# Performance work log

Measured on AMD Instinct MI355X. Metric: run time of the kernel, lower is better.

Reference implementation:

```python
import jax, jax.numpy as jnp
import numpy as np

B, H, T, D = 2, 16, 2048, 64


def setup_inputs() -> dict:
    key = jax.random.key(0)
    kq, kk, kv, km = jax.random.split(key, 4)
    q = jax.random.normal(kq, (B, H, T, D), dtype=jnp.float32)
    k = jax.random.normal(kk, (B, H, T, D), dtype=jnp.float32)
    v = jax.random.normal(kv, (B, H, T, D), dtype=jnp.float32)
    # boolean mask, True = masked out (broadcast over batch and heads)
    mask = jax.random.randint(km, (1, 1, T, T), 0, 2).astype(jnp.bool_)
    return {"q": q, "k": k, "v": v, "mask": mask}


def reference(q, k, v, mask):
    scale = q.shape[-1] ** (-0.5)
    # [B,H,T,T] score matrix (materialized, as in the original)
    scores = jnp.einsum("bhqd,bhkd->bhqk", q, k) * scale
    scores = jnp.where(mask, jnp.float32(-10000.0), scores)
    attn = jax.nn.softmax(scores, axis=-1)
    attn = jnp.where(mask, jnp.float32(0.0), attn)
    return jnp.einsum("bhqk,bhkd->bhqd", attn, v)
```

## Files before the change

kernel.cpp:

```cpp
#include <hip/hip_runtime.h>
#include <hip/hip_bf16.h>

typedef __bf16 bf16x8 __attribute__((ext_vector_type(8)));
typedef __bf16 bf16x4 __attribute__((ext_vector_type(4)));
typedef float  f32x4  __attribute__((ext_vector_type(4)));

#define T_SEQ 2048
#define D_HEAD 64
#define BH_N 32
#define NT_TILES (T_SEQ / 64)
#define QT_N 16
#define IMG_BYTES 16384
#define SCALE_LOG2 0.18033688011112042f

#define WS_IMG ((size_t)0)
#define WS_MB  ((size_t)16u << 20)

static __device__ __forceinline__ f32x4 mfma32(bf16x8 a, bf16x8 b, f32x4 c) {
    return __builtin_amdgcn_mfma_f32_16x16x32_bf16(a, b, c, 0, 0, 0);
}

static __device__ __forceinline__ float fast_exp2(float x) {
#if __has_builtin(__builtin_amdgcn_exp2f)
    return __builtin_amdgcn_exp2f(x);
#else
    return exp2f(x);
#endif
}

static __device__ __forceinline__ void gload16(const void* g, void* l, int lane) {
#if __has_builtin(__builtin_amdgcn_global_load_lds)
    (void)lane;
    __builtin_amdgcn_global_load_lds(
        (const __attribute__((address_space(1))) void*)g,
        (__attribute__((address_space(3))) void*)l, 16, 0, 0);
#else
    *((f32x4*)l + lane) = *(const f32x4*)g;
#endif
}


__global__ __launch_bounds__(256) void prep_kv(const float* __restrict__ k,
                                               const float* __restrict__ v,
                                               char* __restrict__ img) {
    __shared__ __bf16 t[64][72];
    const int bh = blockIdx.y, tt = blockIdx.x, tid = threadIdx.x;
    char* ob = img + ((size_t)bh * NT_TILES + tt) * IMG_BYTES;
    {
        const int kr = tid >> 2, qd = tid & 3, ke = kr & 7;
        const size_t base = ((size_t)bh * T_SEQ + tt * 64 + kr) * D_HEAD + qd * 16;
        const float4 a0 = *(const float4*)(k + base);
        const float4 a1 = *(const float4*)(k + base + 4);
        const float4 a2 = *(const float4*)(k + base + 8);
        const float4 a3 = *(const float4*)(k + base + 12);
        bf16x8 w0, w1;
        w0[0]=(__bf16)a0.x; w0[1]=(__bf16)a0.y; w0[2]=(__bf16)a0.z; w0[3]=(__bf16)a0.w;
        w0[4]=(__bf16)a1.x; w0[5]=(__bf16)a1.y; w0[6]=(__bf16)a1.z; w0[7]=(__bf16)a1.w;
        w1[0]=(__bf16)a2.x; w1[1]=(__bf16)a2.y; w1[2]=(__bf16)a2.z; w1[3]=(__bf16)a2.w;
        w1[4]=(__bf16)a3.x; w1[5]=(__bf16)a3.y; w1[6]=(__bf16)a3.z; w1[7]=(__bf16)a3.w;
        *(bf16x8*)(ob + kr * 128 + (((2 * qd + 0) ^ ke) << 4)) = w0;
        *(bf16x8*)(ob + kr * 128 + (((2 * qd + 1) ^ ke) << 4)) = w1;
    }
    {
        const int tr = tid >> 4, c4 = (tid & 15) * 4;
        const float* src = v + ((size_t)bh * T_SEQ + tt * 64) * D_HEAD;
#pragma unroll
        for (int p = 0; p < 4; ++p) {
            const int row = p * 16 + tr;
            const float4 f = *(const float4*)(src + row * D_HEAD + c4);
            t[c4+0][row] = (__bf16)f.x; t[c4+1][row] = (__bf16)f.y;
            t[c4+2][row] = (__bf16)f.z; t[c4+3][row] = (__bf16)f.w;
        }
        __syncthreads();
        const int d = tid >> 2;
        char* vb = ob + 8192 + d * 128;
#pragma unroll
        for (int mi = 0; mi < 2; ++mi) {
            const int m  = (tid & 3) * 2 + mi;
            const int u  = m ^ (d & 7);
            const int k0 = (u & 1) * 32 + (u >> 1) * 4;
            const bf16x4 lo = *(const bf16x4*)&t[d][k0];
            const bf16x4 hi = *(const bf16x4*)&t[d][k0 + 16];
            *(bf16x8*)(vb + m * 16) = __builtin_shufflevector(lo, hi, 0,1,2,3,4,5,6,7);
        }
    }
}

__global__ void mpack(const int* __restrict__ m, unsigned long long* __restrict__ mb) {
    const int i = blockIdx.x * 256 + threadIdx.x;
    const unsigned long long b = __ballot(m[i] != 0);
    if ((threadIdx.x & 63) == 0) mb[i >> 6] = b;
}


__global__ __launch_bounds__(512, 4) void attn11(
    const float* __restrict__ q, const char* __restrict__ img,
    const unsigned long long* __restrict__ mb, float* __restrict__ out)
{
    const int l   = blockIdx.x;
    const int m_  = l >> 3;
    const int bh  = ((l & 7) << 2) | (m_ & 3);
    const int qt  = m_ >> 2;

    const int tid = threadIdx.x, wave = tid >> 6, lane = tid & 63;
    const int g = lane >> 4, ln = lane & 15;
    const int qp = wave & 3, kh = wave >> 2;

    __shared__ __align__(16) char smem[33280];
    float* Ep = (float*)smem;
    float* Os = (float*)(smem + 32768);

    const int qw = qt * 128 + qp * 32;

    bf16x8 qf[2][2];
#pragma unroll
    for (int qs = 0; qs < 2; ++qs) {
        const float* qpt = q + ((size_t)bh * T_SEQ + qw + qs * 16 + ln) * D_HEAD + g * 8;
#pragma unroll
        for (int kc = 0; kc < 2; ++kc) {
            const float4 f0 = *(const float4*)(qpt + kc * 32);
            const float4 f1 = *(const float4*)(qpt + kc * 32 + 4);
            qf[qs][kc][0]=(__bf16)(f0.x*SCALE_LOG2); qf[qs][kc][1]=(__bf16)(f0.y*SCALE_LOG2);
            qf[qs][kc][2]=(__bf16)(f0.z*SCALE_LOG2); qf[qs][kc][3]=(__bf16)(f0.w*SCALE_LOG2);
            qf[qs][kc][4]=(__bf16)(f1.x*SCALE_LOG2); qf[qs][kc][5]=(__bf16)(f1.y*SCALE_LOG2);
            qf[qs][kc][6]=(__bf16)(f1.z*SCALE_LOG2); qf[qs][kc][7]=(__bf16)(f1.w*SCALE_LOG2);
        }
    }

    f32x4 o[2][4];
#pragma unroll
    for (int qs = 0; qs < 2; ++qs)
#pragma unroll
        for (int mt = 0; mt < 4; ++mt) o[qs][mt] = (f32x4){0.f, 0.f, 0.f, 0.f};
    f32x4 osum[2] = { (f32x4){0.f,0.f,0.f,0.f}, (f32x4){0.f,0.f,0.f,0.f} };
    const bf16x8 ones8 = { (__bf16)1.0f, (__bf16)1.0f, (__bf16)1.0f, (__bf16)1.0f,
                           (__bf16)1.0f, (__bf16)1.0f, (__bf16)1.0f, (__bf16)1.0f };

    const char* ibase = img + (size_t)bh * (NT_TILES * (size_t)IMG_BYTES);
    const unsigned long long* mrow0 = mb + (size_t)(qw + ln) * 32;
    const unsigned long long* mrow1 = mb + (size_t)(qw + 16 + ln) * 32;

    int koffs[2][2];
#pragma unroll
    for (int ntl = 0; ntl < 2; ++ntl) {
        const int row = (2 * kh + ntl) * 16 + ln;
        const int rb = row * 128 + ((g ^ (ln & 7)) << 4);
        koffs[ntl][0] = rb; koffs[ntl][1] = rb ^ 64;
    }
    int voffs[4];
#pragma unroll
    for (int mt = 0; mt < 4; ++mt)
        voffs[mt] = (mt * 16 + ln) * 128 + ((((g << 1) | kh) ^ (ln & 7)) << 4);

    char* buf0 = smem;
    char* buf1 = smem + 16384;

    auto stage = [&](int tile, char* dstbase) {
        const char* src = ibase + (size_t)tile * IMG_BYTES + wave * 2048 + lane * 16;
        char* dst = dstbase + wave * 2048;
        gload16(src, dst, lane);
        gload16(src + 1024, dst + 1024, lane);
    };

    auto compute_tile = [&](const char* KB, const char* VB,
                            unsigned long long w0, unsigned long long w1) {
        const unsigned nbs0 = (~(unsigned)(w0 >> (kh << 5))) >> (g * 4);
        const unsigned nbs1 = (~(unsigned)(w1 >> (kh << 5))) >> (g * 4);

        bf16x8 ka[2][2];
#pragma unroll
        for (int ntl = 0; ntl < 2; ++ntl) {
            ka[ntl][0] = *(const bf16x8*)(KB + koffs[ntl][0]);
            ka[ntl][1] = *(const bf16x8*)(KB + koffs[ntl][1]);
        }

        bf16x8 pa8[2];
#pragma unroll
        for (int ntl = 0; ntl < 2; ++ntl) {
#pragma unroll
            for (int qs = 0; qs < 2; ++qs) {
                f32x4 c = (f32x4){0.f, 0.f, 0.f, 0.f};
                __builtin_amdgcn_s_setprio(1);
                c = mfma32(ka[ntl][0], qf[qs][0], c);
                c = mfma32(ka[ntl][1], qf[qs][1], c);
                __builtin_amdgcn_s_setprio(0);
                const unsigned nbs = qs ? nbs1 : nbs0;
#pragma unroll
                for (int r = 0; r < 4; ++r) {
                    const float e = fast_exp2(c[r]);
                    const int keep = (int)(nbs << (31 - (ntl * 16 + r))) >> 31;
                    const float p = __builtin_bit_cast(float,
                        __builtin_bit_cast(unsigned, e) & (unsigned)keep);
                    pa8[qs][ntl * 4 + r] = (__bf16)p;
                }
            }
        }

        bf16x8 vv[4];
#pragma unroll
        for (int mt = 0; mt < 4; ++mt) vv[mt] = *(const bf16x8*)(VB + voffs[mt]);
        __builtin_amdgcn_s_setprio(1);
#pragma unroll
        for (int qs = 0; qs < 2; ++qs) osum[qs] = mfma32(pa8[qs], ones8, osum[qs]);
#pragma unroll
        for (int mt = 0; mt < 4; ++mt)
#pragma unroll
            for (int qs = 0; qs < 2; ++qs)
                o[qs][mt] = mfma32(pa8[qs], vv[mt], o[qs][mt]);
        __builtin_amdgcn_s_setprio(0);
    };

    stage(0, buf0);
    unsigned long long mwA0 = mrow0[0], mwA1 = mrow1[0];
    __syncthreads();

#pragma unroll 1
    for (int i = 0; i < NT_TILES / 2; ++i) {
        const int t = 2 * i;
        stage(t + 1, buf1);
        const unsigned long long mwB0 = mrow0[t + 1], mwB1 = mrow1[t + 1];
        compute_tile(buf0, buf0 + 8192, mwA0, mwA1);
        __syncthreads();
        if (i < NT_TILES / 2 - 1) {
            stage(t + 2, buf0);
            mwA0 = mrow0[t + 2]; mwA1 = mrow1[t + 2];
        }
        compute_tile(buf1, buf1 + 8192, mwB0, mwB1);
        __syncthreads();
    }

#pragma unroll
    for (int pass = 0; pass < 2; ++pass) {
        if ((qp >> 1) == pass) {
            const int qpl = qp & 1;
#pragma unroll
            for (int qs = 0; qs < 2; ++qs) {
#pragma unroll
                for (int mt = 0; mt < 4; ++mt)
#pragma unroll
                    for (int r = 0; r < 4; ++r)
                        Ep[(size_t)kh * 4096 + (qpl * 32 + qs * 16 + g * 4 + r) * 64 + mt * 16 + ln] = o[qs][mt][r];
                if (ln == 0) {
#pragma unroll
                    for (int r = 0; r < 4; ++r)
                        Os[kh * 64 + qpl * 32 + qs * 16 + g * 4 + r] = osum[qs][r];
                }
            }
        }
        __syncthreads();
#pragma unroll
        for (int p2 = 0; p2 < 2; ++p2) {
            const int idx = p2 * 512 + tid;
            const int row = idx >> 4, c4 = (idx & 15) * 4;
            const float sl = Os[row] + Os[64 + row];
            const float inv = (sl > 0.f) ? (1.f / sl) : 0.f;
            const float4 a  = *(const float4*)(Ep + row * 64 + c4);
            const float4 b4 = *(const float4*)(Ep + 4096 + row * 64 + c4);
            const float4 st = { (a.x + b4.x) * inv, (a.y + b4.y) * inv,
                                (a.z + b4.z) * inv, (a.w + b4.w) * inv };
            *(float4*)(out + ((size_t)bh * T_SEQ + qt * 128 + pass * 64 + row) * D_HEAD + c4) = st;
        }
        if (pass == 0) __syncthreads();
    }
}

extern "C" void kernel_launch(void* const* d_in, const int* in_sizes, int n_in,
                              void* d_out, int out_size, void* d_ws, size_t ws_size,
                              hipStream_t stream) {
    const float* q    = (const float*)d_in[0];
    const float* k    = (const float*)d_in[1];
    const float* v    = (const float*)d_in[2];
    const int*   mask = (const int*)d_in[3];
    float*       out  = (float*)d_out;

    char* img = (char*)d_ws + WS_IMG;
    unsigned long long* mbw = (unsigned long long*)((char*)d_ws + WS_MB);

    prep_kv<<<dim3(NT_TILES, BH_N), 256, 0, stream>>>(k, v, img);
    mpack<<<(T_SEQ * T_SEQ) / 256, 256, 0, stream>>>(mask, mbw);
    attn11<<<dim3(QT_N * BH_N), 512, 0, stream>>>(q, img, mbw, out);
}
```

Measured before the change: 159.5 us.

## Halve query rows per block to double grid size and cut register use

Each block now processes 64 query rows instead of 128, with one 16-row query slice per wave, and the grid doubles. This halves per-wave accumulator and Q-fragment registers and raises the occupancy hint to 8 blocks per CU, aiming for more parallelism and better latency hiding. In exchange, each K/V tile is loaded from global memory and staged into LDS twice as often per output, and each loaded K fragment is reused across fewer MFMAs. The epilogue becomes a single pass.

```diff
diff --git a/kernel.cpp b/kernel.cpp
--- a/kernel.cpp
+++ b/kernel.cpp
@@ -9,7 +9,7 @@
 #define D_HEAD 64
 #define BH_N 32
 #define NT_TILES (T_SEQ / 64)
-#define QT_N 16
+#define QT_N 32
 #define IMG_BYTES 16384
 #define SCALE_LOG2 0.18033688011112042f
 
@@ -93,14 +93,13 @@
 }
 
 
-__global__ __launch_bounds__(512, 4) void attn11(
+__global__ __launch_bounds__(512, 8) void attn12(
     const float* __restrict__ q, const char* __restrict__ img,
     const unsigned long long* __restrict__ mb, float* __restrict__ out)
 {
     const int l   = blockIdx.x;
-    const int m_  = l >> 3;
-    const int bh  = ((l & 7) << 2) | (m_ & 3);
-    const int qt  = m_ >> 2;
+    const int bh  = ((l & 7) << 2) | ((l >> 3) & 3);
+    const int qt  = l >> 5;
 
     const int tid = threadIdx.x, wave = tid >> 6, lane = tid & 63;
     const int g = lane >> 4, ln = lane & 15;
@@ -110,35 +109,31 @@
     float* Ep = (float*)smem;
     float* Os = (float*)(smem + 32768);
 
-    const int qw = qt * 128 + qp * 32;
-
-    bf16x8 qf[2][2];
-#pragma unroll
-    for (int qs = 0; qs < 2; ++qs) {
-        const float* qpt = q + ((size_t)bh * T_SEQ + qw + qs * 16 + ln) * D_HEAD + g * 8;
+    const int qw = qt * 64 + qp * 16;
+
+    bf16x8 qf[2];
+    {
+        const float* qpt = q + ((size_t)bh * T_SEQ + qw + ln) * D_HEAD + g * 8;
 #pragma unroll
         for (int kc = 0; kc < 2; ++kc) {
             const float4 f0 = *(const float4*)(qpt + kc * 32);
             const float4 f1 = *(const float4*)(qpt + kc * 32 + 4);
-            qf[qs][kc][0]=(__bf16)(f0.x*SCALE_LOG2); qf[qs][kc][1]=(__bf16)(f0.y*SCALE_LOG2);
-            qf[qs][kc][2]=(__bf16)(f0.z*SCALE_LOG2); qf[qs][kc][3]=(__bf16)(f0.w*SCALE_LOG2);
-            qf[qs][kc][4]=(__bf16)(f1.x*SCALE_LOG2); qf[qs][kc][5]=(__bf16)(f1.y*SCALE_LOG2);
-            qf[qs][kc][6]=(__bf16)(f1.z*SCALE_LOG2); qf[qs][kc][7]=(__bf16)(f1.w*SCALE_LOG2);
-        }
-    }
-
-    f32x4 o[2][4];
-#pragma unroll
-    for (int qs = 0; qs < 2; ++qs)
-#pragma unroll
-        for (int mt = 0; mt < 4; ++mt) o[qs][mt] = (f32x4){0.f, 0.f, 0.f, 0.f};
-    f32x4 osum[2] = { (f32x4){0.f,0.f,0.f,0.f}, (f32x4){0.f,0.f,0.f,0.f} };
+            qf[kc][0]=(__bf16)(f0.x*SCALE_LOG2); qf[kc][1]=(__bf16)(f0.y*SCALE_LOG2);
+            qf[kc][2]=(__bf16)(f0.z*SCALE_LOG2); qf[kc][3]=(__bf16)(f0.w*SCALE_LOG2);
+            qf[kc][4]=(__bf16)(f1.x*SCALE_LOG2); qf[kc][5]=(__bf16)(f1.y*SCALE_LOG2);
+            qf[kc][6]=(__bf16)(f1.z*SCALE_LOG2); qf[kc][7]=(__bf16)(f1.w*SCALE_LOG2);
+        }
+    }
+
+    f32x4 o[4];
+#pragma unroll
+    for (int mt = 0; mt < 4; ++mt) o[mt] = (f32x4){0.f, 0.f, 0.f, 0.f};
+    f32x4 osum = (f32x4){0.f, 0.f, 0.f, 0.f};
     const bf16x8 ones8 = { (__bf16)1.0f, (__bf16)1.0f, (__bf16)1.0f, (__bf16)1.0f,
                            (__bf16)1.0f, (__bf16)1.0f, (__bf16)1.0f, (__bf16)1.0f };
 
     const char* ibase = img + (size_t)bh * (NT_TILES * (size_t)IMG_BYTES);
-    const unsigned long long* mrow0 = mb + (size_t)(qw + ln) * 32;
-    const unsigned long long* mrow1 = mb + (size_t)(qw + 16 + ln) * 32;
+    const unsigned long long* mrow = mb + (size_t)(qw + ln) * 32;
 
     int koffs[2][2];
 #pragma unroll
@@ -162,105 +157,80 @@
         gload16(src + 1024, dst + 1024, lane);
     };
 
-    auto compute_tile = [&](const char* KB, const char* VB,
-                            unsigned long long w0, unsigned long long w1) {
-        const unsigned nbs0 = (~(unsigned)(w0 >> (kh << 5))) >> (g * 4);
-        const unsigned nbs1 = (~(unsigned)(w1 >> (kh << 5))) >> (g * 4);
-
-        bf16x8 ka[2][2];
+    auto compute_tile = [&](const char* KB, const char* VB, unsigned long long w0) {
+        const unsigned nbs = (~(unsigned)(w0 >> (kh << 5))) >> (g * 4);
+
+        bf16x8 pa8;
 #pragma unroll
         for (int ntl = 0; ntl < 2; ++ntl) {
-            ka[ntl][0] = *(const bf16x8*)(KB + koffs[ntl][0]);
-            ka[ntl][1] = *(const bf16x8*)(KB + koffs[ntl][1]);
-        }
-
-        bf16x8 pa8[2];
-#pragma unroll
-        for (int ntl = 0; ntl < 2; ++ntl) {
-#pragma unroll
-            for (int qs = 0; qs < 2; ++qs) {
-                f32x4 c = (f32x4){0.f, 0.f, 0.f, 0.f};
-                __builtin_amdgcn_s_setprio(1);
-                c = mfma32(ka[ntl][0], qf[qs][0], c);
-                c = mfma32(ka[ntl][1], qf[qs][1], c);
-                __builtin_amdgcn_s_setprio(0);
-                const unsigned nbs = qs ? nbs1 : nbs0;
-#pragma unroll
-                for (int r = 0; r < 4; ++r) {
-                    const float e = fast_exp2(c[r]);
-                    const int keep = (int)(nbs << (31 - (ntl * 16 + r))) >> 31;
-                    const float p = __builtin_bit_cast(float,
-                        __builtin_bit_cast(unsigned, e) & (unsigned)keep);
-                    pa8[qs][ntl * 4 + r] = (__bf16)p;
-                }
+            const bf16x8 a0 = *(const bf16x8*)(KB + koffs[ntl][0]);
+            const bf16x8 a1 = *(const bf16x8*)(KB + koffs[ntl][1]);
+            f32x4 c = (f32x4){0.f, 0.f, 0.f, 0.f};
+            __builtin_amdgcn_s_setprio(1);
+            c = mfma32(a0, qf[0], c);
+            c = mfma32(a1, qf[1], c);
+            __builtin_amdgcn_s_setprio(0);
+#pragma unroll
+            for (int r = 0; r < 4; ++r) {
+                const float e = fast_exp2(c[r]);
+                const int keep = (int)(nbs << (31 - (ntl * 16 + r))) >> 31;
+                const float p = __builtin_bit_cast(float,
+                    __builtin_bit_cast(unsigned, e) & (unsigned)keep);
+                pa8[ntl * 4 + r] = (__bf16)p;
             }
         }
 
-        bf16x8 vv[4];
-#pragma unroll
-        for (int mt = 0; mt < 4; ++mt) vv[mt] = *(const bf16x8*)(VB + voffs[mt]);
         __builtin_amdgcn_s_setprio(1);
-#pragma unroll
-        for (int qs = 0; qs < 2; ++qs) osum[qs] = mfma32(pa8[qs], ones8, osum[qs]);
-#pragma unroll
-        for (int mt = 0; mt < 4; ++mt)
-#pragma unroll
-            for (int qs = 0; qs < 2; ++qs)
-                o[qs][mt] = mfma32(pa8[qs], vv[mt], o[qs][mt]);
+        osum = mfma32(pa8, ones8, osum);
+#pragma unroll
+        for (int mt = 0; mt < 4; ++mt) {
+            const bf16x8 vv = *(const bf16x8*)(VB + voffs[mt]);
+            o[mt] = mfma32(pa8, vv, o[mt]);
+        }
         __builtin_amdgcn_s_setprio(0);
     };
 
     stage(0, buf0);
-    unsigned long long mwA0 = mrow0[0], mwA1 = mrow1[0];
+    unsigned long long mwA = mrow[0];
     __syncthreads();
 
 #pragma unroll 1
     for (int i = 0; i < NT_TILES / 2; ++i) {
         const int t = 2 * i;
         stage(t + 1, buf1);
-        const unsigned long long mwB0 = mrow0[t + 1], mwB1 = mrow1[t + 1];
-        compute_tile(buf0, buf0 + 8192, mwA0, mwA1);
+        const unsigned long long mwB = mrow[t + 1];
+        compute_tile(buf0, buf0 + 8192, mwA);
         __syncthreads();
         if (i < NT_TILES / 2 - 1) {
             stage(t + 2, buf0);
-            mwA0 = mrow0[t + 2]; mwA1 = mrow1[t + 2];
-        }
-        compute_tile(buf1, buf1 + 8192, mwB0, mwB1);
+            mwA = mrow[t + 2];
+        }
+        compute_tile(buf1, buf1 + 8192, mwB);
         __syncthreads();
     }
 
 #pragma unroll
-    for (int pass = 0; pass < 2; ++pass) {
-        if ((qp >> 1) == pass) {
-            const int qpl = qp & 1;
-#pragma unroll
-            for (int qs = 0; qs < 2; ++qs) {
-#pragma unroll
-                for (int mt = 0; mt < 4; ++mt)
-#pragma unroll
-                    for (int r = 0; r < 4; ++r)
-                        Ep[(size_t)kh * 4096 + (qpl * 32 + qs * 16 + g * 4 + r) * 64 + mt * 16 + ln] = o[qs][mt][r];
-                if (ln == 0) {
-#pragma unroll
-                    for (int r = 0; r < 4; ++r)
-                        Os[kh * 64 + qpl * 32 + qs * 16 + g * 4 + r] = osum[qs][r];
-                }
-            }
-        }
-        __syncthreads();
-#pragma unroll
-        for (int p2 = 0; p2 < 2; ++p2) {
-            const int idx = p2 * 512 + tid;
-            const int row = idx >> 4, c4 = (idx & 15) * 4;
-            const float sl = Os[row] + Os[64 + row];
-            const float inv = (sl > 0.f) ? (1.f / sl) : 0.f;
-            const float4 a  = *(const float4*)(Ep + row * 64 + c4);
-            const float4 b4 = *(const float4*)(Ep + 4096 + row * 64 + c4);
-            const float4 st = { (a.x + b4.x) * inv, (a.y + b4.y) * inv,
-                                (a.z + b4.z) * inv, (a.w + b4.w) * inv };
-            *(float4*)(out + ((size_t)bh * T_SEQ + qt * 128 + pass * 64 + row) * D_HEAD + c4) = st;
-        }
-        if (pass == 0) __syncthreads();
+    for (int mt = 0; mt < 4; ++mt)
+#pragma unroll
+        for (int r = 0; r < 4; ++r)
+            Ep[(size_t)kh * 4096 + (qp * 16 + g * 4 + r) * 64 + mt * 16 + ln] = o[mt][r];
+    if (ln == 0) {
+#pragma unroll
+        for (int r = 0; r < 4; ++r)
+            Os[kh * 64 + qp * 16 + g * 4 + r] = osum[r];
+    }
+    __syncthreads();
+#pragma unroll
+    for (int p2 = 0; p2 < 2; ++p2) {
+        const int idx = p2 * 512 + tid;
+        const int row = idx >> 4, c4 = (idx & 15) * 4;
+        const float sl = Os[row] + Os[64 + row];
+        const float inv = (sl > 0.f) ? (1.f / sl) : 0.f;
+        const float4 a  = *(const float4*)(Ep + row * 64 + c4);
+        const float4 b4 = *(const float4*)(Ep + 4096 + row * 64 + c4);
+        const float4 st = { (a.x + b4.x) * inv, (a.y + b4.y) * inv,
+                            (a.z + b4.z) * inv, (a.w + b4.w) * inv };
+        *(float4*)(out + ((size_t)bh * T_SEQ + qt * 64 + row) * D_HEAD + c4) = st;
     }
 }
 
@@ -278,5 +248,5 @@
 
     prep_kv<<<dim3(NT_TILES, BH_N), 256, 0, stream>>>(k, v, img);
     mpack<<<(T_SEQ * T_SEQ) / 256, 256, 0, stream>>>(mask, mbw);
-    attn11<<<dim3(QT_N * BH_N), 512, 0, stream>>>(q, img, mbw, out);
-}
+    attn12<<<dim3(QT_N * BH_N), 512, 0, stream>>>(q, img, mbw, out);
+}
```

After: 166.2 us. 1.04x slower.

## Software-pipeline PV matmul of previous tile with QK and softmax of current tile

Applied to the files above, without the earlier changes.

Splits the per-tile compute into QK, softmax, V-read and PV stages and reorders them so the PV MFMAs of the previous tile are issued right after the QK MFMAs of the current tile. This is meant to let exp/mask ALU work overlap MFMA execution, hiding dependency latency within a wave. It keeps the probabilities and V fragments live across iterations, which raises register pressure under the 4-waves launch bound and adds a prologue and epilogue.

```diff
diff --git a/kernel.cpp b/kernel.cpp
--- a/kernel.cpp
+++ b/kernel.cpp
@@ -93,7 +93,7 @@
 }
 
 
-__global__ __launch_bounds__(512, 4) void attn11(
+__global__ __launch_bounds__(512, 4) void attn13(
     const float* __restrict__ q, const char* __restrict__ img,
     const unsigned long long* __restrict__ mb, float* __restrict__ out)
 {
@@ -155,6 +155,9 @@
     char* buf0 = smem;
     char* buf1 = smem + 16384;
 
+    bf16x8 pa8_p[2];
+    bf16x8 vv_p[4];
+
     auto stage = [&](int tile, char* dstbase) {
         const char* src = ibase + (size_t)tile * IMG_BYTES + wave * 2048 + lane * 16;
         char* dst = dstbase + wave * 2048;
@@ -162,72 +165,109 @@
         gload16(src + 1024, dst + 1024, lane);
     };
 
-    auto compute_tile = [&](const char* KB, const char* VB,
-                            unsigned long long w0, unsigned long long w1) {
+    auto QK = [&](const char* KB, f32x4 (&c)[2][2]) {
+#pragma unroll
+        for (int ntl = 0; ntl < 2; ++ntl) {
+            const bf16x8 a0 = *(const bf16x8*)(KB + koffs[ntl][0]);
+            const bf16x8 a1 = *(const bf16x8*)(KB + koffs[ntl][1]);
+            __builtin_amdgcn_s_setprio(1);
+#pragma unroll
+            for (int qs = 0; qs < 2; ++qs) {
+                f32x4 t0 = (f32x4){0.f, 0.f, 0.f, 0.f};
+                t0 = mfma32(a0, qf[qs][0], t0);
+                t0 = mfma32(a1, qf[qs][1], t0);
+                c[ntl][qs] = t0;
+            }
+            __builtin_amdgcn_s_setprio(0);
+        }
+    };
+
+    auto PVV = [&]() {
+        __builtin_amdgcn_s_setprio(1);
+#pragma unroll
+        for (int qs = 0; qs < 2; ++qs) osum[qs] = mfma32(pa8_p[qs], ones8, osum[qs]);
+#pragma unroll
+        for (int mt = 0; mt < 4; ++mt)
+#pragma unroll
+            for (int qs = 0; qs < 2; ++qs)
+                o[qs][mt] = mfma32(pa8_p[qs], vv_p[mt], o[qs][mt]);
+        __builtin_amdgcn_s_setprio(0);
+    };
+
+    auto SOFT = [&](const f32x4 (&c)[2][2], unsigned long long w0, unsigned long long w1) {
         const unsigned nbs0 = (~(unsigned)(w0 >> (kh << 5))) >> (g * 4);
         const unsigned nbs1 = (~(unsigned)(w1 >> (kh << 5))) >> (g * 4);
-
-        bf16x8 ka[2][2];
-#pragma unroll
-        for (int ntl = 0; ntl < 2; ++ntl) {
-            ka[ntl][0] = *(const bf16x8*)(KB + koffs[ntl][0]);
-            ka[ntl][1] = *(const bf16x8*)(KB + koffs[ntl][1]);
-        }
-
-        bf16x8 pa8[2];
-#pragma unroll
-        for (int ntl = 0; ntl < 2; ++ntl) {
+#pragma unroll
+        for (int ntl = 0; ntl < 2; ++ntl)
 #pragma unroll
             for (int qs = 0; qs < 2; ++qs) {
-                f32x4 c = (f32x4){0.f, 0.f, 0.f, 0.f};
-                __builtin_amdgcn_s_setprio(1);
-                c = mfma32(ka[ntl][0], qf[qs][0], c);
-                c = mfma32(ka[ntl][1], qf[qs][1], c);
-                __builtin_amdgcn_s_setprio(0);
                 const unsigned nbs = qs ? nbs1 : nbs0;
 #pragma unroll
                 for (int r = 0; r < 4; ++r) {
-                    const float e = fast_exp2(c[r]);
+                    const float e = fast_exp2(c[ntl][qs][r]);
                     const int keep = (int)(nbs << (31 - (ntl * 16 + r))) >> 31;
                     const float p = __builtin_bit_cast(float,
                         __builtin_bit_cast(unsigned, e) & (unsigned)keep);
-                    pa8[qs][ntl * 4 + r] = (__bf16)p;
+                    pa8_p[qs][ntl * 4 + r] = (__bf16)p;
                 }
             }
-        }
-
-        bf16x8 vv[4];
-#pragma unroll
-        for (int mt = 0; mt < 4; ++mt) vv[mt] = *(const bf16x8*)(VB + voffs[mt]);
-        __builtin_amdgcn_s_setprio(1);
-#pragma unroll
-        for (int qs = 0; qs < 2; ++qs) osum[qs] = mfma32(pa8[qs], ones8, osum[qs]);
-#pragma unroll
-        for (int mt = 0; mt < 4; ++mt)
-#pragma unroll
-            for (int qs = 0; qs < 2; ++qs)
-                o[qs][mt] = mfma32(pa8[qs], vv[mt], o[qs][mt]);
-        __builtin_amdgcn_s_setprio(0);
+    };
+
+    auto VREAD = [&](const char* KB) {
+        const char* VB = KB + 8192;
+#pragma unroll
+        for (int mt = 0; mt < 4; ++mt) vv_p[mt] = *(const bf16x8*)(VB + voffs[mt]);
     };
 
     stage(0, buf0);
-    unsigned long long mwA0 = mrow0[0], mwA1 = mrow1[0];
     __syncthreads();
 
+    {
+        stage(1, buf1);
+        const unsigned long long w0 = mrow0[0], w1 = mrow1[0];
+        f32x4 c[2][2];
+        QK(buf0, c);
+        SOFT(c, w0, w1);
+        VREAD(buf0);
+        __syncthreads();
+    }
+
 #pragma unroll 1
-    for (int i = 0; i < NT_TILES / 2; ++i) {
-        const int t = 2 * i;
-        stage(t + 1, buf1);
-        const unsigned long long mwB0 = mrow0[t + 1], mwB1 = mrow1[t + 1];
-        compute_tile(buf0, buf0 + 8192, mwA0, mwA1);
+    for (int i = 0; i < 15; ++i) {
+        {
+            const int t = 2 * i + 1;
+            stage(t + 1, buf0);
+            const unsigned long long w0 = mrow0[t], w1 = mrow1[t];
+            f32x4 c[2][2];
+            QK(buf1, c);
+            PVV();
+            SOFT(c, w0, w1);
+            VREAD(buf1);
+            __syncthreads();
+        }
+        {
+            const int t = 2 * i + 2;
+            stage(t + 1, buf1);
+            const unsigned long long w0 = mrow0[t], w1 = mrow1[t];
+            f32x4 c[2][2];
+            QK(buf0, c);
+            PVV();
+            SOFT(c, w0, w1);
+            VREAD(buf0);
+            __syncthreads();
+        }
+    }
+
+    {
+        const unsigned long long w0 = mrow0[31], w1 = mrow1[31];
+        f32x4 c[2][2];
+        QK(buf1, c);
+        PVV();
+        SOFT(c, w0, w1);
+        VREAD(buf1);
         __syncthreads();
-        if (i < NT_TILES / 2 - 1) {
-            stage(t + 2, buf0);
-            mwA0 = mrow0[t + 2]; mwA1 = mrow1[t + 2];
-        }
-        compute_tile(buf1, buf1 + 8192, mwB0, mwB1);
-        __syncthreads();
-    }
+    }
+    PVV();
 
 #pragma unroll
     for (int pass = 0; pass < 2; ++pass) {
@@ -278,5 +318,5 @@
 
     prep_kv<<<dim3(NT_TILES, BH_N), 256, 0, stream>>>(k, v, img);
     mpack<<<(T_SEQ * T_SEQ) / 256, 256, 0, stream>>>(mask, mbw);
-    attn11<<<dim3(QT_N * BH_N), 512, 0, stream>>>(q, img, mbw, out);
-}
+    attn13<<<dim3(QT_N * BH_N), 512, 0, stream>>>(q, img, mbw, out);
+}
```

Measured after the change: 162.6 us. Within noise of the previous version (+1.9%).
